# Kernel optimization log

Hardware: AMD Instinct MI355X
Metric: run time of the kernel (lower is better)

## Reference

```python
import jax, jax.numpy as jnp
import numpy as np

N, E, F_IN, G = 100000, 1600000, 128, 64
H1, H2, H3 = 64, 32, 16


def _xavier(key, fan_in, fan_out):
    lim = np.sqrt(6.0 / (fan_in + fan_out))
    return jax.random.uniform(key, (fan_in, fan_out), jnp.float32, -lim, lim)


def setup_inputs() -> dict:
    key = jax.random.key(0)
    ks = jax.random.split(key, 16)
    x = jax.random.normal(ks[0], (N, F_IN), jnp.float32)
    edge_index = jax.random.randint(ks[1], (2, E), 0, N, dtype=jnp.int32)
    batch = jnp.sort(jax.random.randint(ks[2], (N,), 0, G, dtype=jnp.int32))
    d = {
        "x": x,
        "W1": _xavier(ks[3], F_IN, H1), "b1": jnp.zeros((H1,), jnp.float32),
        "W2": _xavier(ks[4], H1, H2), "b2": jnp.zeros((H2,), jnp.float32),
        "W3": _xavier(ks[5], H2, H3), "b3": jnp.zeros((H3,), jnp.float32),
        "g1": jnp.ones((H1,), jnp.float32), "be1": jnp.zeros((H1,), jnp.float32),
        "g2": jnp.ones((H2,), jnp.float32), "be2": jnp.zeros((H2,), jnp.float32),
        "g3": jnp.ones((H3,), jnp.float32), "be3": jnp.zeros((H3,), jnp.float32),
        "attn_w": _xavier(ks[6], 3 * H3, 3), "attn_b": jnp.zeros((3,), jnp.float32),
        "fc1_w": _xavier(ks[7], H3, H3), "fc1_b": jnp.zeros((H3,), jnp.float32),
        "fc2_w": _xavier(ks[8], H3, H3 // 2), "fc2_b": jnp.zeros((H3 // 2,), jnp.float32),
        "out_w": _xavier(ks[9], H3 // 2, 1), "out_b": jnp.zeros((1,), jnp.float32),
        "edge_index": edge_index,
        "batch": batch,
        "num_graphs": G,
    }
    return d


def _lrelu(z):
    return jnp.where(z > 0, z, 0.1 * z)


def _bn(h, gamma, beta, eps=1e-5):
    # BatchNorm1d forward with batch statistics (biased variance), as torch training-mode math
    m = jnp.mean(h, axis=0)
    v = jnp.mean(jnp.square(h - m), axis=0)
    return (h - m) * jax.lax.rsqrt(v + eps) * gamma + beta


def reference(x, W1, b1, W2, b2, W3, b3, g1, be1, g2, be2, g3, be3,
              attn_w, attn_b, fc1_w, fc1_b, fc2_w, fc2_b, out_w, out_b,
              edge_index, batch, num_graphs):
    src, dst = edge_index[0], edge_index[1]
    n = x.shape[0]
    # GCN degree with self-loops: deg[i] = 1 + #incoming edges
    deg = jax.ops.segment_sum(jnp.ones((src.shape[0],), x.dtype), dst, num_segments=n) + 1.0
    dis = jax.lax.rsqrt(deg)                      # deg^-1/2, [N]
    enorm = dis[src] * dis[dst]                   # per-edge norm, [E]
    selfw = dis * dis                             # self-loop norm, [N]

    def gcn(h, W, b):
        hw = h @ W                                # [N, H]
        agg = jax.ops.segment_sum(hw[src] * enorm[:, None], dst, num_segments=n)
        return agg + selfw[:, None] * hw + b

    x1 = _lrelu(_bn(gcn(x, W1, b1), g1, be1))     # dropout = identity (eval)
    x2 = _lrelu(_bn(gcn(x1, W2, b2), g2, be2))    # residual skipped: 64 != 32
    x3 = _lrelu(_bn(gcn(x2, W3, b3), g3, be3))    # residual skipped: 32 != 16

    # multi-pool over graphs
    ones_n = jnp.ones((n,), x.dtype)
    counts = jax.ops.segment_sum(ones_n, batch, num_segments=num_graphs)  # [G]
    x_sum = jax.ops.segment_sum(x3, batch, num_segments=num_graphs)       # [G, H3]
    x_mean = x_sum / jnp.maximum(counts, 1.0)[:, None]
    x_max = jax.ops.segment_max(x3, batch, num_segments=num_graphs)

    pooled = jnp.concatenate([x_mean, x_max, x_sum], axis=1)              # [G, 3*H3]
    aw = jax.nn.softmax(pooled @ attn_w + attn_b, axis=1)                 # [G, 3]
    xg = aw[:, 0:1] * x_mean + aw[:, 1:2] * x_max + aw[:, 2:3] * x_sum    # [G, H3]

    xg = _lrelu(xg @ fc1_w + fc1_b)
    xg = _lrelu(xg @ fc2_w + fc2_b)
    out = jax.nn.sigmoid(xg @ out_w + out_b)                              # [G, 1]
    return out
```

## Files before the change

kernel.cpp:

```cpp
#include <hip/hip_runtime.h>

#define GG 64
#define SREP 32
#define BSH 14
typedef unsigned long long ull;
typedef unsigned short u16;
typedef unsigned int uint;

__device__ __forceinline__ u16 f2b(float x) {
    unsigned u = __float_as_uint(x);
    return (u16)((u + 0x7FFFu + ((u >> 16) & 1u)) >> 16);
}

__device__ __forceinline__ void add8(const uint4 q, float* acc) {
    acc[0] += __uint_as_float(q.x << 16);
    acc[1] += __uint_as_float(q.x & 0xFFFF0000u);
    acc[2] += __uint_as_float(q.y << 16);
    acc[3] += __uint_as_float(q.y & 0xFFFF0000u);
    acc[4] += __uint_as_float(q.z << 16);
    acc[5] += __uint_as_float(q.z & 0xFFFF0000u);
    acc[6] += __uint_as_float(q.w << 16);
    acc[7] += __uint_as_float(q.w & 0xFFFF0000u);
}

__global__ __launch_bounds__(256) void k_hist(const int* __restrict__ src,
                                              const int* __restrict__ dst,
                                              int* __restrict__ cnt4, int E, int n) {
    const int part = blockIdx.x & 7;
    const int nblk = gridDim.x >> 3;
    const int bser = blockIdx.x >> 3;
    const int lo = (int)(((long long)part * n) >> 3);
    const int hi = (part == 7) ? n : (int)(((long long)(part + 1) * n) >> 3);
    for (int e = bser * 256 + threadIdx.x; e < E; e += nblk * 256) {
        int d = dst[e];
        if (d >= lo && d < hi) {
            int b = min(src[e] >> BSH, 7);
            atomicAdd(&cnt4[(d << 3) + b], 1);
        }
    }
}

__global__ void k_sum4(const int* __restrict__ cnt4, int* __restrict__ cnt,
                       float* __restrict__ dis, int n) {
    int i = blockIdx.x * blockDim.x + threadIdx.x;
    if (i < n) {
        int t = 0;
        #pragma unroll
        for (int b = 0; b < 8; ++b) t += cnt4[(i << 3) + b];
        cnt[i] = t;
        dis[i] = rsqrtf((float)t + 1.0f);
    }
}

__global__ void k_scanA(const int* __restrict__ cnt, int* __restrict__ rp,
                        int* __restrict__ bsum, int n) {
    __shared__ int s[256];
    int i = blockIdx.x * 256 + threadIdx.x;
    int v = (i < n) ? cnt[i] : 0;
    s[threadIdx.x] = v;
    __syncthreads();
    for (int off = 1; off < 256; off <<= 1) {
        int t = (threadIdx.x >= off) ? s[threadIdx.x - off] : 0;
        __syncthreads();
        s[threadIdx.x] += t;
        __syncthreads();
    }
    if (i < n) rp[i] = s[threadIdx.x] - v;
    if (threadIdx.x == 255) bsum[blockIdx.x] = s[255];
}

__global__ void k_scanB(int* __restrict__ bsum, int nb) {
    __shared__ int s[512];
    int v = (threadIdx.x < nb) ? bsum[threadIdx.x] : 0;
    s[threadIdx.x] = v;
    __syncthreads();
    for (int off = 1; off < 512; off <<= 1) {
        int t = (threadIdx.x >= off) ? s[threadIdx.x - off] : 0;
        __syncthreads();
        s[threadIdx.x] += t;
        __syncthreads();
    }
    if (threadIdx.x < nb) bsum[threadIdx.x] = s[threadIdx.x] - v;
}

__global__ void k_scanC(int* __restrict__ rp, const int* __restrict__ bsum,
                        const int* __restrict__ cnt4, int* __restrict__ cursor4,
                        int n, int E) {
    int i = blockIdx.x * 256 + threadIdx.x;
    if (i < n) {
        int r = rp[i] + bsum[blockIdx.x];
        rp[i] = r;
        int run = r;
        #pragma unroll
        for (int b = 0; b < 8; ++b) {
            cursor4[(i << 3) + b] = run;
            run += cnt4[(i << 3) + b];
        }
    }
    if (i == 0) rp[n] = E;
}

__global__ __launch_bounds__(256) void k_scatter(const int* __restrict__ src,
                                                 const int* __restrict__ dst,
                                                 int* __restrict__ cursor4,
                                                 uint* __restrict__ epack, int E, int n) {
    const int part = blockIdx.x & 7;
    const int nblk = gridDim.x >> 3;
    const int bser = blockIdx.x >> 3;
    const int lo = (int)(((long long)part * n) >> 3);
    const int hi = (part == 7) ? n : (int)(((long long)(part + 1) * n) >> 3);
    for (int e = bser * 256 + threadIdx.x; e < E; e += nblk * 256) {
        int d = dst[e];
        if (d >= lo && d < hi) {
            int s = src[e];
            int b = min(s >> BSH, 7);
            int pos = atomicAdd(&cursor4[(d << 3) + b], 1);
            epack[pos] = (uint)s;
        }
    }
}

template <int FIN, int FOUT, bool BN>
__global__ __launch_bounds__(256) void k_mm(const float* __restrict__ h,
                                            const float* __restrict__ W,
                                            const float* __restrict__ dis,
                                            const float* __restrict__ stats,
                                            const float* __restrict__ gma,
                                            const float* __restrict__ bta,
                                            u16* __restrict__ hw, int n) {
    constexpr int FX  = FOUT / 4;
    constexpr int TY  = 256 / FX;
    constexpr int NT  = TY * 4;
    constexpr int LDA = FIN + ((FOUT == 64) ? 2 : 1);
    __shared__ float sA[NT * LDA];
    __shared__ float sW[FIN * FOUT];
    __shared__ float sSc[FIN], sSh[FIN];

    if (BN && threadIdx.x < FIN) {
        int f = threadIdx.x;
        float s = 0.f, q = 0.f;
        #pragma unroll 8
        for (int r = 0; r < SREP; ++r) {
            s += stats[(r << 7) + f];
            q += stats[(r << 7) + 64 + f];
        }
        float inv_n = 1.0f / (float)n;
        float m = s * inv_n;
        float var = fmaxf(q * inv_n - m * m, 0.f);
        float sc = rsqrtf(var + 1e-5f) * gma[f];
        sSc[f] = sc;
        sSh[f] = bta[f] - m * sc;
    }
    for (int i = threadIdx.x; i < FIN * FOUT / 4; i += 256)
        ((float4*)sW)[i] = ((const float4*)W)[i];
    if (BN) __syncthreads();

    const int node0 = blockIdx.x * NT;
    constexpr int LD4 = NT * FIN / 4 / 256;
    #pragma unroll
    for (int i = 0; i < LD4; ++i) {
        int idx4 = i * 256 + threadIdx.x;
        int row = idx4 / (FIN / 4);
        int c4  = idx4 % (FIN / 4);
        int gn  = node0 + row;
        float4 v = make_float4(0.f, 0.f, 0.f, 0.f);
        if (gn < n) v = ((const float4*)(h + (long long)gn * FIN))[c4];
        if (BN) {
            int f = c4 * 4;
            float t;
            t = fmaf(v.x, sSc[f + 0], sSh[f + 0]); v.x = t > 0.f ? t : 0.1f * t;
            t = fmaf(v.y, sSc[f + 1], sSh[f + 1]); v.y = t > 0.f ? t : 0.1f * t;
            t = fmaf(v.z, sSc[f + 2], sSh[f + 2]); v.z = t > 0.f ? t : 0.1f * t;
            t = fmaf(v.w, sSc[f + 3], sSh[f + 3]); v.w = t > 0.f ? t : 0.1f * t;
        }
        float* p = &sA[row * LDA + c4 * 4];
        p[0] = v.x; p[1] = v.y; p[2] = v.z; p[3] = v.w;
    }
    __syncthreads();

    const int tx = threadIdx.x % FX;
    const int ty = threadIdx.x / FX;
    float acc[4][4];
    #pragma unroll
    for (int i = 0; i < 4; ++i)
        #pragma unroll
        for (int j = 0; j < 4; ++j) acc[i][j] = 0.f;

    #pragma unroll 8
    for (int k = 0; k < FIN; ++k) {
        float4 wv = *((const float4*)&sW[k * FOUT + tx * 4]);
        float a0 = sA[(ty * 4 + 0) * LDA + k];
        float a1 = sA[(ty * 4 + 1) * LDA + k];
        float a2 = sA[(ty * 4 + 2) * LDA + k];
        float a3 = sA[(ty * 4 + 3) * LDA + k];
        acc[0][0] = fmaf(a0, wv.x, acc[0][0]); acc[0][1] = fmaf(a0, wv.y, acc[0][1]);
        acc[0][2] = fmaf(a0, wv.z, acc[0][2]); acc[0][3] = fmaf(a0, wv.w, acc[0][3]);
        acc[1][0] = fmaf(a1, wv.x, acc[1][0]); acc[1][1] = fmaf(a1, wv.y, acc[1][1]);
        acc[1][2] = fmaf(a1, wv.z, acc[1][2]); acc[1][3] = fmaf(a1, wv.w, acc[1][3]);
        acc[2][0] = fmaf(a2, wv.x, acc[2][0]); acc[2][1] = fmaf(a2, wv.y, acc[2][1]);
        acc[2][2] = fmaf(a2, wv.z, acc[2][2]); acc[2][3] = fmaf(a2, wv.w, acc[2][3]);
        acc[3][0] = fmaf(a3, wv.x, acc[3][0]); acc[3][1] = fmaf(a3, wv.y, acc[3][1]);
        acc[3][2] = fmaf(a3, wv.z, acc[3][2]); acc[3][3] = fmaf(a3, wv.w, acc[3][3]);
    }

    #pragma unroll
    for (int i = 0; i < 4; ++i) {
        int gn = node0 + ty * 4 + i;
        if (gn < n) {
            float dv = dis[gn];
            ushort4 o;
            o.x = f2b(acc[i][0] * dv); o.y = f2b(acc[i][1] * dv);
            o.z = f2b(acc[i][2] * dv); o.w = f2b(acc[i][3] * dv);
            ((ushort4*)(hw + (long long)gn * FOUT))[tx] = o;
        }
    }
}

template <int FOUT, int T>
__global__ __launch_bounds__(256) void k_aggt(const u16* __restrict__ hwb,
                                              const uint* __restrict__ epack,
                                              const int* __restrict__ rp,
                                              const int* __restrict__ cursor4,
                                              const float* __restrict__ dis,
                                              const float* __restrict__ bias,
                                              float* __restrict__ y,
                                              float* __restrict__ stats,
                                              int n, int nbuck) {
    constexpr int LPN = FOUT / 8;
    constexpr int GPB = 256 / LPN;
    constexpr int NPB = GPB * T;
    constexpr int RS  = FOUT / 8;
    __shared__ float ssum[FOUT], ssq[FOUT];
    for (int i = threadIdx.x; i < FOUT; i += 256) { ssum[i] = 0.f; ssq[i] = 0.f; }
    __syncthreads();
    const int grp = threadIdx.x / LPN;
    const int fq  = threadIdx.x % LPN;
    const uint4* hw4 = (const uint4*)hwb;

    int nd[T], jp[T];
    float acc[T][8];
    #pragma unroll
    for (int t = 0; t < T; ++t) {
        nd[t] = blockIdx.x * NPB + grp * T + t;
        jp[t] = (nd[t] < n) ? rp[nd[t]] : 0;
        #pragma unroll
        for (int i = 0; i < 8; ++i) acc[t][i] = 0.f;
    }

    for (int b = 0; b < nbuck; ++b) {
        int je[T];
        #pragma unroll
        for (int t = 0; t < T; ++t)
            je[t] = (nd[t] < n) ? cursor4[(nd[t] << 3) + b] : 0;
        bool more = (jp[0] < je[0]);
        #pragma unroll
        for (int t = 1; t < T; ++t) more |= (jp[t] < je[t]);
        while (more) {
            more = false;
            uint idx[T];
            bool act[T];
            #pragma unroll
            for (int t = 0; t < T; ++t) {
                act[t] = jp[t] < je[t];
                idx[t] = epack[act[t] ? jp[t] : 0];
            }
            uint4 q[T];
            #pragma unroll
            for (int t = 0; t < T; ++t) {
                int row = act[t] ? (int)idx[t] : min(nd[t], n - 1);
                q[t] = hw4[(long long)row * RS + fq];
            }
            #pragma unroll
            for (int t = 0; t < T; ++t) {
                if (act[t]) {
                    add8(q[t], acc[t]);
                    ++jp[t];
                    more |= (jp[t] < je[t]);
                }
            }
        }
    }

    float lsum[8] = {0,0,0,0,0,0,0,0}, lsq[8] = {0,0,0,0,0,0,0,0};
    float b8[8];
    #pragma unroll
    for (int i = 0; i < 8; ++i) b8[i] = bias[fq * 8 + i];
    #pragma unroll
    for (int t = 0; t < T; ++t) {
        int node = nd[t];
        if (node < n) {
            uint4 qs = hw4[(long long)node * RS + fq];
            add8(qs, acc[t]);
            float dv = dis[node];
            #pragma unroll
            for (int i = 0; i < 8; ++i) acc[t][i] = fmaf(dv, acc[t][i], b8[i]);
            float4* y4 = (float4*)y;
            long long o = (long long)node * (FOUT / 4) + fq * 2;
            y4[o]     = make_float4(acc[t][0], acc[t][1], acc[t][2], acc[t][3]);
            y4[o + 1] = make_float4(acc[t][4], acc[t][5], acc[t][6], acc[t][7]);
            #pragma unroll
            for (int i = 0; i < 8; ++i) {
                lsum[i] += acc[t][i];
                lsq[i] = fmaf(acc[t][i], acc[t][i], lsq[i]);
            }
        }
    }
    #pragma unroll
    for (int i = 0; i < 8; ++i) {
        atomicAdd(&ssum[fq * 8 + i], lsum[i]);
        atomicAdd(&ssq[fq * 8 + i], lsq[i]);
    }
    __syncthreads();
    float* st = stats + ((blockIdx.x & (SREP - 1)) << 7);
    for (int i = threadIdx.x; i < FOUT; i += 256) {
        atomicAdd(&st[i], ssum[i]);
        atomicAdd(&st[64 + i], ssq[i]);
    }
}

template <int FOUT>
__global__ __launch_bounds__(256) void k_agg(const u16* __restrict__ hwb,
                                             const uint* __restrict__ epack,
                                             const int* __restrict__ rp,
                                             const float* __restrict__ dis,
                                             const float* __restrict__ bias,
                                             float* __restrict__ y,
                                             float* __restrict__ stats, int n) {
    constexpr int LPN = FOUT / 8;
    constexpr int NPB = 256 / LPN;
    constexpr int RS  = FOUT / 8;
    __shared__ float ssum[FOUT], ssq[FOUT];
    for (int i = threadIdx.x; i < FOUT; i += 256) { ssum[i] = 0.f; ssq[i] = 0.f; }
    __syncthreads();
    const int local = threadIdx.x / LPN;
    const int fq = threadIdx.x % LPN;
    const uint4* hw4 = (const uint4*)hwb;
    float b8[8];
    #pragma unroll
    for (int i = 0; i < 8; ++i) b8[i] = bias[fq * 8 + i];
    float lsum[8] = {0,0,0,0,0,0,0,0}, lsq[8] = {0,0,0,0,0,0,0,0};

    int node = blockIdx.x * NPB + local;
    if (node < n) {
        int j0 = rp[node], j1 = rp[node + 1];
        float acc[8] = {0,0,0,0,0,0,0,0};
        int j = j0;
        for (; j + 8 <= j1; j += 8) {
            uint s0 = epack[j + 0], s1 = epack[j + 1], s2 = epack[j + 2], s3 = epack[j + 3];
            uint s4 = epack[j + 4], s5 = epack[j + 5], s6 = epack[j + 6], s7 = epack[j + 7];
            uint4 q0 = hw4[(long long)s0 * RS + fq];
            uint4 q1 = hw4[(long long)s1 * RS + fq];
            uint4 q2 = hw4[(long long)s2 * RS + fq];
            uint4 q3 = hw4[(long long)s3 * RS + fq];
            uint4 q4 = hw4[(long long)s4 * RS + fq];
            uint4 q5 = hw4[(long long)s5 * RS + fq];
            uint4 q6 = hw4[(long long)s6 * RS + fq];
            uint4 q7 = hw4[(long long)s7 * RS + fq];
            add8(q0, acc); add8(q1, acc); add8(q2, acc); add8(q3, acc);
            add8(q4, acc); add8(q5, acc); add8(q6, acc); add8(q7, acc);
        }
        for (; j + 2 <= j1; j += 2) {
            uint s0 = epack[j + 0], s1 = epack[j + 1];
            uint4 q0 = hw4[(long long)s0 * RS + fq];
            uint4 q1 = hw4[(long long)s1 * RS + fq];
            add8(q0, acc); add8(q1, acc);
        }
        for (; j < j1; ++j) {
            uint4 q = hw4[(long long)epack[j] * RS + fq];
            add8(q, acc);
        }
        uint4 qs = hw4[(long long)node * RS + fq];
        add8(qs, acc);
        float dv = dis[node];
        #pragma unroll
        for (int i = 0; i < 8; ++i) acc[i] = fmaf(dv, acc[i], b8[i]);
        float4* y4 = (float4*)y;
        long long o = (long long)node * (FOUT / 4) + fq * 2;
        y4[o]     = make_float4(acc[0], acc[1], acc[2], acc[3]);
        y4[o + 1] = make_float4(acc[4], acc[5], acc[6], acc[7]);
        #pragma unroll
        for (int i = 0; i < 8; ++i) {
            lsum[i] += acc[i];
            lsq[i] = fmaf(acc[i], acc[i], lsq[i]);
        }
    }
    #pragma unroll
    for (int i = 0; i < 8; ++i) {
        atomicAdd(&ssum[fq * 8 + i], lsum[i]);
        atomicAdd(&ssq[fq * 8 + i], lsq[i]);
    }
    __syncthreads();
    float* st = stats + ((blockIdx.x & (SREP - 1)) << 7);
    for (int i = threadIdx.x; i < FOUT; i += 256) {
        atomicAdd(&st[i], ssum[i]);
        atomicAdd(&st[64 + i], ssq[i]);
    }
}

__global__ void k_pool_graph(const float* __restrict__ yraw, const int* __restrict__ batch,
                             const float* __restrict__ stats, const float* __restrict__ gma,
                             const float* __restrict__ bta, int n,
                             float* __restrict__ psum, float* __restrict__ pmax,
                             float* __restrict__ pcnt) {
    const int g = blockIdx.x;
    const int f = threadIdx.x & 15;
    float s = 0.f, q = 0.f;
    #pragma unroll 8
    for (int r = 0; r < SREP; ++r) {
        s += stats[(r << 7) + f];
        q += stats[(r << 7) + 64 + f];
    }
    float inv_n = 1.0f / (float)n;
    float m = s * inv_n;
    float var = fmaxf(q * inv_n - m * m, 0.f);
    float sc = rsqrtf(var + 1e-5f) * gma[f];
    float sh = bta[f] - m * sc;

    __shared__ int s_lo, s_hi;
    if (threadIdx.x == 0) {
        int lo = 0, hi = n;
        while (lo < hi) { int mid = (lo + hi) >> 1; if (batch[mid] < g) lo = mid + 1; else hi = mid; }
        s_lo = lo;
        hi = n;
        while (lo < hi) { int mid = (lo + hi) >> 1; if (batch[mid] < g + 1) lo = mid + 1; else hi = mid; }
        s_hi = lo;
    }
    __syncthreads();
    const int start = s_lo, end = s_hi;
    float lsum = 0.f, lmax = -3.0e38f;
    for (long long idx = (long long)start * 16 + threadIdx.x; idx < (long long)end * 16; idx += blockDim.x) {
        float t = fmaf(yraw[idx], sc, sh);
        float v = t > 0.f ? t : 0.1f * t;
        lsum += v;
        lmax = fmaxf(lmax, v);
    }
    __shared__ float ss[256], sm[256];
    ss[threadIdx.x] = lsum; sm[threadIdx.x] = lmax;
    __syncthreads();
    for (int off = 128; off >= 16; off >>= 1) {
        if (threadIdx.x < off) {
            ss[threadIdx.x] += ss[threadIdx.x + off];
            sm[threadIdx.x] = fmaxf(sm[threadIdx.x], sm[threadIdx.x + off]);
        }
        __syncthreads();
    }
    if (threadIdx.x < 16) {
        psum[g * 16 + threadIdx.x] = ss[threadIdx.x];
        pmax[g * 16 + threadIdx.x] = sm[threadIdx.x];
    }
    if (threadIdx.x == 0) pcnt[g] = (float)(end - start);
}

__global__ void k_head(const float* __restrict__ psum, const float* __restrict__ pmax,
                       const float* __restrict__ pcnt,
                       const float* __restrict__ attn_w, const float* __restrict__ attn_b,
                       const float* __restrict__ fc1_w, const float* __restrict__ fc1_b,
                       const float* __restrict__ fc2_w, const float* __restrict__ fc2_b,
                       const float* __restrict__ out_w, const float* __restrict__ out_b,
                       float* __restrict__ out) {
    int g = threadIdx.x;
    if (g >= GG) return;
    float xs[16], xm[16], xx[16];
    float c = fmaxf(pcnt[g], 1.0f);
    for (int f = 0; f < 16; ++f) {
        xs[f] = psum[(g << 4) + f];
        xm[f] = xs[f] / c;
        xx[f] = pmax[(g << 4) + f];
    }
    float lg[3];
    for (int cI = 0; cI < 3; ++cI) {
        float a = attn_b[cI];
        for (int f = 0; f < 16; ++f) {
            a += xm[f] * attn_w[f * 3 + cI];
            a += xx[f] * attn_w[(16 + f) * 3 + cI];
            a += xs[f] * attn_w[(32 + f) * 3 + cI];
        }
        lg[cI] = a;
    }
    float mx = fmaxf(lg[0], fmaxf(lg[1], lg[2]));
    float e0 = expf(lg[0] - mx), e1 = expf(lg[1] - mx), e2 = expf(lg[2] - mx);
    float inv = 1.0f / (e0 + e1 + e2);
    float a0 = e0 * inv, a1 = e1 * inv, a2 = e2 * inv;
    float xg[16];
    for (int f = 0; f < 16; ++f) xg[f] = a0 * xm[f] + a1 * xx[f] + a2 * xs[f];
    float t1[16];
    for (int j = 0; j < 16; ++j) {
        float a = fc1_b[j];
        for (int k = 0; k < 16; ++k) a += xg[k] * fc1_w[k * 16 + j];
        t1[j] = a > 0.f ? a : 0.1f * a;
    }
    float t2[8];
    for (int j = 0; j < 8; ++j) {
        float a = fc2_b[j];
        for (int k = 0; k < 16; ++k) a += t1[k] * fc2_w[k * 8 + j];
        t2[j] = a > 0.f ? a : 0.1f * a;
    }
    float o = out_b[0];
    for (int k = 0; k < 8; ++k) o += t2[k] * out_w[k];
    o = 1.0f / (1.0f + expf(-o));
    out[g] = o;
}

extern "C" void kernel_launch(void* const* d_in, const int* in_sizes, int n_in,
                              void* d_out, int out_size, void* d_ws, size_t ws_size,
                              hipStream_t stream) {
    const float* x      = (const float*)d_in[0];
    const float* W1     = (const float*)d_in[1];  const float* b1   = (const float*)d_in[2];
    const float* W2     = (const float*)d_in[3];  const float* b2   = (const float*)d_in[4];
    const float* W3     = (const float*)d_in[5];  const float* b3   = (const float*)d_in[6];
    const float* g1     = (const float*)d_in[7];  const float* be1  = (const float*)d_in[8];
    const float* g2     = (const float*)d_in[9];  const float* be2  = (const float*)d_in[10];
    const float* g3     = (const float*)d_in[11]; const float* be3  = (const float*)d_in[12];
    const float* attn_w = (const float*)d_in[13]; const float* attn_b = (const float*)d_in[14];
    const float* fc1_w  = (const float*)d_in[15]; const float* fc1_b  = (const float*)d_in[16];
    const float* fc2_w  = (const float*)d_in[17]; const float* fc2_b  = (const float*)d_in[18];
    const float* out_w  = (const float*)d_in[19]; const float* out_b  = (const float*)d_in[20];
    const int* edge_index = (const int*)d_in[21];
    const int* batch      = (const int*)d_in[22];

    const int N = in_sizes[0] / 128;
    const int E = in_sizes[21] / 2;
    const int* srcp = edge_index;
    const int* dstp = edge_index + E;
    const int nb = (N + 255) / 256;
    const int NBUCK = min((N + (1 << BSH) - 1) >> BSH, 8);

    char* ws = (char*)d_ws;
    float* dis    = (float*)(ws);
    int*   cnt    = (int*)(ws + 0x80000);
    int*   rp     = (int*)(ws + 0x100000);
    int*   bsum   = (int*)(ws + 0x180000);
    float* stats1 = (float*)(ws + 0x180800);
    float* stats2 = (float*)(ws + 0x184800);
    float* stats3 = (float*)(ws + 0x188800);
    float* psum   = (float*)(ws + 0x18C800);
    float* pmax   = (float*)(ws + 0x18D800);
    float* pcnt   = (float*)(ws + 0x18E800);
    int*   cnt4    = (int*)(ws + 0x190000);
    int*   cursor4 = cnt4 + (size_t)8 * N;
    uint*  epack   = (uint*)(cursor4 + (size_t)8 * N);
    float* buf1    = (float*)((char*)epack + (((size_t)E * 4 + 255) & ~(size_t)255));
    u16*   hwb     = (u16*)(buf1 + (size_t)N * 64);

    hipMemsetAsync(cnt4, 0, (size_t)N * 32, stream);
    k_hist<<<2048, 256, 0, stream>>>(srcp, dstp, cnt4, E, N);
    k_sum4<<<nb, 256, 0, stream>>>(cnt4, cnt, dis, N);
    k_scanA<<<nb, 256, 0, stream>>>(cnt, rp, bsum, N);
    k_scanB<<<1, 512, 0, stream>>>(bsum, nb);
    k_scanC<<<nb, 256, 0, stream>>>(rp, bsum, cnt4, cursor4, N, E);
    k_scatter<<<2048, 256, 0, stream>>>(srcp, dstp, cursor4, epack, E, N);
    hipMemsetAsync(stats1, 0, 3 * SREP * 512, stream);

    k_mm<128, 64, false><<<(N + 63) / 64, 256, 0, stream>>>(
        x, W1, dis, nullptr, nullptr, nullptr, hwb, N);
    k_aggt<64, 4><<<(N + 127) / 128, 256, 0, stream>>>(
        hwb, epack, rp, cursor4, dis, b1, buf1, stats1, N, NBUCK);

    k_mm<64, 32, true><<<(N + 127) / 128, 256, 0, stream>>>(
        buf1, W2, dis, stats1, g1, be1, hwb, N);
    k_aggt<32, 4><<<(N + 255) / 256, 256, 0, stream>>>(
        hwb, epack, rp, cursor4, dis, b2, buf1, stats2, N, NBUCK);

    k_mm<32, 16, true><<<(N + 255) / 256, 256, 0, stream>>>(
        buf1, W3, dis, stats2, g2, be2, hwb, N);
    k_agg<16><<<(N + 127) / 128, 256, 0, stream>>>(hwb, epack, rp, dis, b3, buf1, stats3, N);

    k_pool_graph<<<GG, 256, 0, stream>>>(buf1, batch, stats3, g3, be3, N, psum, pmax, pcnt);
    k_head<<<1, 64, 0, stream>>>(psum, pmax, pcnt, attn_w, attn_b,
                                 fc1_w, fc1_b, fc2_w, fc2_b, out_w, out_b,
                                 (float*)d_out);
}
```

Baseline: 552.5 us.

## Prefetch next bucket rows in aggregation and split graph pooling across blocks

In the bucketed aggregation kernel, each block cooperatively loads a slice of the next source-row bucket of hw into registers before handling the current bucket. An empty asm statement keeps those loads alive so the rows are warm in L2 when the next bucket is gathered. Graph pooling now uses 8 blocks per graph instead of 1, writing partial sums, maxes and counts that the head kernel combines. The partial buffers move to the workspace slot that held cnt, which is free by then. The trade-off is extra register pressure and bandwidth from the prefetch loads, plus a little more work in the head kernel.

```diff
diff --git a/kernel.cpp b/kernel.cpp
--- a/kernel.cpp
+++ b/kernel.cpp
@@ -248,6 +248,29 @@
     }
 
     for (int b = 0; b < nbuck; ++b) {
+        uint4 pf0 = make_uint4(0,0,0,0), pf1 = pf0, pf2 = pf0,
+              pf3 = pf0, pf4 = pf0, pf5 = pf0;
+        if (b + 1 < nbuck) {
+            long long base = (long long)(b + 1) << BSH;
+            long long rows = (long long)n - base;
+            if (rows > (1LL << BSH)) rows = 1LL << BSH;
+            if (rows > 0) {
+                long long tU4 = rows * RS;
+                int xidx = (int)(blockIdx.x >> 3);
+                int nX   = (int)((gridDim.x + 7) >> 3);
+                long long u0 = tU4 * xidx / nX;
+                long long u1 = tU4 * (xidx + 1) / nX;
+                const uint4* tb = hw4 + base * RS;
+                long long i = u0 + threadIdx.x;
+                if (i < u1) { pf0 = tb[i]; i += 256; }
+                if (i < u1) { pf1 = tb[i]; i += 256; }
+                if (i < u1) { pf2 = tb[i]; i += 256; }
+                if (i < u1) { pf3 = tb[i]; i += 256; }
+                if (i < u1) { pf4 = tb[i]; i += 256; }
+                if (i < u1) { pf5 = tb[i]; }
+            }
+        }
+
         int je[T];
         #pragma unroll
         for (int t = 0; t < T; ++t)
@@ -279,6 +302,8 @@
                 }
             }
         }
+        asm volatile("" :: "v"(pf0.x), "v"(pf1.x), "v"(pf2.x),
+                           "v"(pf3.x), "v"(pf4.x), "v"(pf5.x));
     }
 
     float lsum[8] = {0,0,0,0,0,0,0,0}, lsq[8] = {0,0,0,0,0,0,0,0};
@@ -402,7 +427,8 @@
                              const float* __restrict__ bta, int n,
                              float* __restrict__ psum, float* __restrict__ pmax,
                              float* __restrict__ pcnt) {
-    const int g = blockIdx.x;
+    const int g    = blockIdx.x >> 3;
+    const int part = blockIdx.x & 7;
     const int f = threadIdx.x & 15;
     float s = 0.f, q = 0.f;
     #pragma unroll 8
@@ -426,7 +452,9 @@
         s_hi = lo;
     }
     __syncthreads();
-    const int start = s_lo, end = s_hi;
+    const int gs = s_lo, len = s_hi - s_lo;
+    const int start = gs + (int)(((long long)len * part) >> 3);
+    const int end   = gs + (int)(((long long)len * (part + 1)) >> 3);
     float lsum = 0.f, lmax = -3.0e38f;
     for (long long idx = (long long)start * 16 + threadIdx.x; idx < (long long)end * 16; idx += blockDim.x) {
         float t = fmaf(yraw[idx], sc, sh);
@@ -445,10 +473,10 @@
         __syncthreads();
     }
     if (threadIdx.x < 16) {
-        psum[g * 16 + threadIdx.x] = ss[threadIdx.x];
-        pmax[g * 16 + threadIdx.x] = sm[threadIdx.x];
-    }
-    if (threadIdx.x == 0) pcnt[g] = (float)(end - start);
+        psum[(((g << 3) + part) << 4) + threadIdx.x] = ss[threadIdx.x];
+        pmax[(((g << 3) + part) << 4) + threadIdx.x] = sm[threadIdx.x];
+    }
+    if (threadIdx.x == 0) pcnt[(g << 3) + part] = (float)(end - start);
 }
 
 __global__ void k_head(const float* __restrict__ psum, const float* __restrict__ pmax,
@@ -461,12 +489,17 @@
     int g = threadIdx.x;
     if (g >= GG) return;
     float xs[16], xm[16], xx[16];
-    float c = fmaxf(pcnt[g], 1.0f);
-    for (int f = 0; f < 16; ++f) {
-        xs[f] = psum[(g << 4) + f];
-        xm[f] = xs[f] / c;
-        xx[f] = pmax[(g << 4) + f];
-    }
+    float c = 0.f;
+    for (int p = 0; p < 8; ++p) c += pcnt[(g << 3) + p];
+    c = fmaxf(c, 1.0f);
+    for (int f = 0; f < 16; ++f) { xs[f] = 0.f; xx[f] = -3.0e38f; }
+    for (int p = 0; p < 8; ++p) {
+        for (int f = 0; f < 16; ++f) {
+            xs[f] += psum[(((g << 3) + p) << 4) + f];
+            xx[f] = fmaxf(xx[f], pmax[(((g << 3) + p) << 4) + f]);
+        }
+    }
+    for (int f = 0; f < 16; ++f) xm[f] = xs[f] / c;
     float lg[3];
     for (int cI = 0; cI < 3; ++cI) {
         float a = attn_b[cI];
@@ -533,9 +566,9 @@
     float* stats1 = (float*)(ws + 0x180800);
     float* stats2 = (float*)(ws + 0x184800);
     float* stats3 = (float*)(ws + 0x188800);
-    float* psum   = (float*)(ws + 0x18C800);
-    float* pmax   = (float*)(ws + 0x18D800);
-    float* pcnt   = (float*)(ws + 0x18E800);
+    float* psum   = (float*)(ws + 0x80000);
+    float* pmax   = psum + GG * 8 * 16;
+    float* pcnt   = pmax + GG * 8 * 16;
     int*   cnt4    = (int*)(ws + 0x190000);
     int*   cursor4 = cnt4 + (size_t)8 * N;
     uint*  epack   = (uint*)(cursor4 + (size_t)8 * N);
@@ -565,7 +598,7 @@
         buf1, W3, dis, stats2, g2, be2, hwb, N);
     k_agg<16><<<(N + 127) / 128, 256, 0, stream>>>(hwb, epack, rp, dis, b3, buf1, stats3, N);
 
-    k_pool_graph<<<GG, 256, 0, stream>>>(buf1, batch, stats3, g3, be3, N, psum, pmax, pcnt);
+    k_pool_graph<<<GG * 8, 256, 0, stream>>>(buf1, batch, stats3, g3, be3, N, psum, pmax, pcnt);
     k_head<<<1, 64, 0, stream>>>(psum, pmax, pcnt, attn_w, attn_b,
                                  fc1_w, fc1_b, fc2_w, fc2_b, out_w, out_b,
                                  (float*)d_out);
```

Result: faster. 534.0 us (-3.4%).
